# Kernel tuning notes

Measured on AMD Instinct MI355X. Metric: run time of the kernel, lower is better.

Reference implementation:

```python
import jax, jax.numpy as jnp
import numpy as np
import math

HEADS = 8
EMBED = 512
HEAD_DIM = EMBED // HEADS
N, L = 2, 256


def setup_inputs() -> dict:
    key = jax.random.key(0)
    ks = jax.random.split(key, 16)
    s = 0.05  # weight scale for numerical stability
    inp = {
        "values": jax.random.normal(ks[0], (N, L, EMBED), jnp.float32),
        "keys": jax.random.normal(ks[1], (N, L, EMBED), jnp.float32),
        "query": jax.random.normal(ks[2], (N, L, EMBED), jnp.float32),
        "pos": jax.random.normal(ks[3], (N, L, EMBED), jnp.float32),
        "rel": jax.random.normal(ks[4], (N, L, L, EMBED), jnp.float32),
        "mask": jnp.ones((N, L), jnp.float32),
        "Wv": jax.random.normal(ks[5], (HEAD_DIM, HEAD_DIM), jnp.float32) * s,
        "Wk": jax.random.normal(ks[6], (HEAD_DIM, HEAD_DIM), jnp.float32) * s,
        "Wq": jax.random.normal(ks[7], (HEAD_DIM, HEAD_DIM), jnp.float32) * s,
        "Wpq": jax.random.normal(ks[8], (HEAD_DIM, HEAD_DIM), jnp.float32) * s,
        "Wpk": jax.random.normal(ks[9], (HEAD_DIM, HEAD_DIM), jnp.float32) * s,
        "Wrk": jax.random.normal(ks[10], (HEAD_DIM, HEAD_DIM), jnp.float32) * s,
        "Wrq": jax.random.normal(ks[11], (HEAD_DIM, HEAD_DIM), jnp.float32) * s,
        "Wout": jax.random.normal(ks[12], (EMBED, EMBED), jnp.float32) * s,
        "bout": jnp.zeros((EMBED,), jnp.float32),
    }
    return inp


def reference(values, keys, query, pos, rel, mask, Wv, Wk, Wq, Wpq, Wpk, Wrk, Wrq, Wout, bout):
    n, lq, e = query.shape
    h, d = HEADS, e // HEADS
    # split heads; per-head Linear shares one [d,d] weight (y = x @ W.T)
    v = values.reshape(n, -1, h, d) @ Wv.T
    k = keys.reshape(n, -1, h, d) @ Wk.T
    q = query.reshape(n, lq, h, d) @ Wq.T
    p = pos.reshape(n, lq, h, d)
    r = rel.reshape(n, lq, lq, h, d)
    # mode == 'all': QK + pos-pos + two relative terms
    scores = jnp.einsum('nqhd,nkhd->nhqk', q, k)
    pq = p @ Wpq.T
    pk = p @ Wpk.T
    pos_scores = jnp.einsum('nqhd,nkhd->nhqk', pq, pk)
    rk = r @ Wrk.T
    rq = r @ Wrq.T
    rel1 = jnp.einsum('nqhd,nqkhd->nhqk', q, rk)
    rel2 = jnp.einsum('nqkhd,nkhd->nhqk', rq, k)
    energy = (scores + pos_scores + rel1 + rel2) / math.sqrt(2.0)
    energy = energy + (1.0 - mask)[:, None, None, :] * (-1e9)
    attn = jax.nn.softmax(energy, axis=3)
    out = jnp.einsum('nhqk,nkhd->nqhd', attn, v).reshape(n, lq, e)
    return out @ Wout.T + bout
```

## Files before the change

### kernel.cpp

```cpp
#include <hip/hip_runtime.h>
#include <hip/hip_bf16.h>

#define NB 2
#define L 256
#define H 8
#define D 64
#define E 512
#define NL (NB * L)
#define RSQRT2 0.70710678118654752f

__global__ __launch_bounds__(256) void k0_transpose(const float* __restrict__ Wout,
                                                    float* __restrict__ WoutT) {
    __shared__ float tile[64][65];
    int t = threadIdx.x;
    int bi = blockIdx.x >> 3;
    int bj = blockIdx.x & 7;
    int tx = t & 63, ty = t >> 6;
#pragma unroll
    for (int m = 0; m < 16; m++) {
        int el = ty + (m << 2);
        tile[el][tx] = Wout[(size_t)(bi * 64 + el) * E + bj * 64 + tx];
    }
    __syncthreads();
#pragma unroll
    for (int m = 0; m < 16; m++) {
        int cl = ty + (m << 2);
        WoutT[(size_t)(bj * 64 + cl) * E + bi * 64 + tx] = tile[tx][cl];
    }
}

__device__ __forceinline__ float dot64(const float* __restrict__ a,
                                       const float* __restrict__ w) {
    const float4* a4 = (const float4*)a;
    const float4* w4 = (const float4*)w;
    float acc = 0.f;
#pragma unroll
    for (int j = 0; j < 16; j++) {
        float4 x = a4[j], y = w4[j];
        acc = fmaf(x.x, y.x, acc);
        acc = fmaf(x.y, y.y, acc);
        acc = fmaf(x.z, y.z, acc);
        acc = fmaf(x.w, y.w, acc);
    }
    return acc;
}

__global__ __launch_bounds__(256) void k1_proj(
    const float* __restrict__ values, const float* __restrict__ keys,
    const float* __restrict__ query, const float* __restrict__ pos,
    const float* __restrict__ Wv, const float* __restrict__ Wk,
    const float* __restrict__ Wq, const float* __restrict__ Wpq,
    const float* __restrict__ Wpk, const float* __restrict__ Wrk,
    const float* __restrict__ Wrq,
    float* __restrict__ qv_ws, float* __restrict__ kv_ws,
    float* __restrict__ vv_ws, float* __restrict__ pq_ws,
    float* __restrict__ pk_ws, float* __restrict__ qrk_ws,
    float* __restrict__ krq_ws) {
    __shared__ float xq[E], xk[E], xv[E], xp[E];
    __shared__ float qs[E], ks[E];
    int t = threadIdx.x;
    int nl = blockIdx.x;
    size_t base = (size_t)nl * E;
    for (int j = t; j < E; j += 256) {
        xq[j] = query[base + j];
        xk[j] = keys[base + j];
        xv[j] = values[base + j];
        xp[j] = pos[base + j];
    }
    __syncthreads();
#pragma unroll
    for (int cc = 0; cc < 2; cc++) {
        int c = t + cc * 256;
        int h = c >> 6, i = c & 63;
        const float* xqh = xq + (h << 6);
        const float* xkh = xk + (h << 6);
        const float* xvh = xv + (h << 6);
        const float* xph = xp + (h << 6);
        float q_c = dot64(xqh, Wq + (i << 6));
        float k_c = dot64(xkh, Wk + (i << 6));
        float v_c = dot64(xvh, Wv + (i << 6));
        float pq_c = dot64(xph, Wpq + (i << 6));
        float pk_c = dot64(xph, Wpk + (i << 6));
        qv_ws[base + c] = q_c;
        kv_ws[base + c] = k_c;
        vv_ws[base + c] = v_c;
        pq_ws[base + c] = pq_c;
        pk_ws[base + c] = pk_c;
        qs[c] = q_c;
        ks[c] = k_c;
    }
    __syncthreads();
#pragma unroll
    for (int cc = 0; cc < 2; cc++) {
        int c = t + cc * 256;
        int h = c >> 6, d = c & 63;
        float aq = 0.f, ak = 0.f;
        const float* qh = qs + (h << 6);
        const float* kh = ks + (h << 6);
#pragma unroll 8
        for (int i = 0; i < 64; i++) {
            aq = fmaf(qh[i], Wrk[(i << 6) + d], aq);
            ak = fmaf(kh[i], Wrq[(i << 6) + d], ak);
        }
        qrk_ws[base + c] = aq;
        krq_ws[base + c] = ak;
    }
}

__global__ __launch_bounds__(256) void k2pre(
    const float* __restrict__ qv_ws, const float* __restrict__ kv_ws,
    const float* __restrict__ pq_ws, const float* __restrict__ pk_ws,
    const float* __restrict__ mask, float* __restrict__ e_ws) {
    __shared__ float qs[8 * 64], ps[8 * 64];
    int t = threadIdx.x;
    int b = blockIdx.x;
    int qt = b & 31;
    int h = (b >> 5) & 7;
    int n = b >> 8;
    int nb = n << 8;
    int q0 = qt << 3;
    int k = t;
#pragma unroll
    for (int it = 0; it < 2; it++) {
        int idx = t + (it << 8);
        int q = idx >> 6, d = idx & 63;
        size_t g = (size_t)(nb + q0 + q) * E + (h << 6) + d;
        qs[idx] = qv_ws[g];
        ps[idx] = pq_ws[g];
    }
    __syncthreads();
    const float4* kv4p = (const float4*)(kv_ws + (size_t)(nb + k) * E + (h << 6));
    const float4* pk4p = (const float4*)(pk_ws + (size_t)(nb + k) * E + (h << 6));
    float acc[8];
#pragma unroll
    for (int q = 0; q < 8; q++) acc[q] = 0.f;
#pragma unroll
    for (int d4 = 0; d4 < 16; d4++) {
        float4 kv4 = kv4p[d4];
        float4 pk4 = pk4p[d4];
#pragma unroll
        for (int q = 0; q < 8; q++) {
            float4 q4 = ((const float4*)qs)[(q << 4) + d4];
            float4 p4 = ((const float4*)ps)[(q << 4) + d4];
            float a = acc[q];
            a = fmaf(q4.x, kv4.x, a);
            a = fmaf(q4.y, kv4.y, a);
            a = fmaf(q4.z, kv4.z, a);
            a = fmaf(q4.w, kv4.w, a);
            a = fmaf(p4.x, pk4.x, a);
            a = fmaf(p4.y, pk4.y, a);
            a = fmaf(p4.z, pk4.z, a);
            a = fmaf(p4.w, pk4.w, a);
            acc[q] = a;
        }
    }
    float mk = (1.0f - mask[nb + k]) * (-1e9f);
#pragma unroll
    for (int q = 0; q < 8; q++) {
        e_ws[(size_t)(nb + q0 + q) * (H * L) + (h << 8) + k] = acc[q] * RSQRT2 + mk;
    }
}


#define K2REL_LOAD(R, QK, qi_)                                                  \
    do {                                                                        \
        const int gq_ = nbase + q0 + (qi_);                                     \
        const float* relb_ =                                                    \
            rel + (size_t)gq_ * (size_t)(L * E) + (size_t)kb * E + cq;          \
        _Pragma("unroll") for (int jj = 0; jj < 8; jj++)                        \
            R[jj] = *(const float4*)(relb_ + (size_t)((jj << 1) + rowsel) * E); \
        QK = *(const float4*)(qrk_ws + (size_t)gq_ * E + cq);                   \
    } while (0)

#define K2REL_COMP(R, QK, qi_)                                                  \
    do {                                                                        \
        const int gq_ = nbase + q0 + (qi_);                                     \
        float* rb_ = r_ws + (size_t)gq_ * (H * L) + (h << 8);                   \
        _Pragma("unroll") for (int jj = 0; jj < 8; jj++) {                      \
            float wx = QK.x + kq[jj].x;                                         \
            float wy = QK.y + kq[jj].y;                                         \
            float wz = QK.z + kq[jj].z;                                         \
            float ww = QK.w + kq[jj].w;                                         \
            float p = R[jj].x * wx;                                             \
            p = fmaf(R[jj].y, wy, p);                                           \
            p = fmaf(R[jj].z, wz, p);                                           \
            p = fmaf(R[jj].w, ww, p);                                           \
            p += __shfl_down(p, 8, 16);                                         \
            p += __shfl_down(p, 4, 16);                                         \
            p += __shfl_down(p, 2, 16);                                         \
            p += __shfl_down(p, 1, 16);                                         \
            if (sub == 0) rb_[kb + (jj << 1) + rowsel] = p * RSQRT2;            \
        }                                                                       \
    } while (0)

__global__ __launch_bounds__(256, 2) void k2rel(
    const float* __restrict__ rel, const float* __restrict__ qrk_ws,
    const float* __restrict__ krq_ws, float* __restrict__ r_ws) {
    int t = threadIdx.x;
    int b = blockIdx.x;
    int kc = b & 15;
    int qt = (b >> 4) & 15;
    int n = b >> 8;

    int lane128 = t & 127;
    int rowsel = t >> 7;
    int cq = lane128 << 2;
    int h = lane128 >> 4;
    int sub = t & 15;
    int nbase = n << 8;
    int kb = kc << 4;
    int q0 = qt << 4;

    float4 kq[8];
#pragma unroll
    for (int jj = 0; jj < 8; jj++) {
        kq[jj] = *(const float4*)(krq_ws +
                                  (size_t)(nbase + kb + (jj << 1) + rowsel) * E + cq);
    }

    float4 rA[8], rB[8], rC[8], rD[8];
    float4 qA, qB, qC, qD;
    K2REL_LOAD(rA, qA, 0);
    K2REL_LOAD(rB, qB, 1);
    K2REL_LOAD(rC, qC, 2);
#pragma unroll
    for (int qi = 0; qi < 16; qi += 4) {
        K2REL_LOAD(rD, qD, qi + 3);
        K2REL_COMP(rA, qA, qi);
        if (qi < 12) K2REL_LOAD(rA, qA, qi + 4);
        K2REL_COMP(rB, qB, qi + 1);
        if (qi < 12) K2REL_LOAD(rB, qB, qi + 5);
        K2REL_COMP(rC, qC, qi + 2);
        if (qi < 12) K2REL_LOAD(rC, qC, qi + 6);
        K2REL_COMP(rD, qD, qi + 3);
    }
}

__global__ __launch_bounds__(512) void k2b_soft_av(
    const float* __restrict__ e_ws, const float* __restrict__ r_ws,
    const float* __restrict__ vv_ws, float* __restrict__ attn_ws) {
    __shared__ float e_s[H * L];
    __shared__ float PS[4 * E];
    __shared__ float inv_s[H];
    int t = threadIdx.x;
    int nq = blockIdx.x;
    int n = nq >> 8;

    {
        float4 a = ((const float4*)(e_ws + (size_t)nq * (H * L)))[t];
        float4 b = ((const float4*)(r_ws + (size_t)nq * (H * L)))[t];
        a.x += b.x; a.y += b.y; a.z += b.z; a.w += b.w;
        ((float4*)e_s)[t] = a;
    }
    __syncthreads();

    {
        int hh = t >> 6;
        int lane = t & 63;
        float* eh = e_s + (hh << 8);
        float m = -INFINITY;
#pragma unroll
        for (int j = 0; j < 4; j++) m = fmaxf(m, eh[lane + (j << 6)]);
#pragma unroll
        for (int off = 32; off > 0; off >>= 1) m = fmaxf(m, __shfl_xor(m, off, 64));
        float s = 0.f;
#pragma unroll
        for (int j = 0; j < 4; j++) {
            int idx = lane + (j << 6);
            float ev = __expf(eh[idx] - m);
            eh[idx] = ev;
            s += ev;
        }
#pragma unroll
        for (int off = 32; off > 0; off >>= 1) s += __shfl_xor(s, off, 64);
        if (lane == 0) inv_s[hh] = 1.0f / s;
    }
    __syncthreads();

    {
        int c4 = (t & 127) << 2;
        int kseg = t >> 7;
        int h1 = c4 >> 6;
        const float* eh = e_s + (h1 << 8) + (kseg << 6);
        const float* vb = vv_ws + ((size_t)(n << 8) + (kseg << 6)) * E + c4;
        float4 acc = {0.f, 0.f, 0.f, 0.f};
#pragma unroll 16
        for (int k = 0; k < 64; k++) {
            float ev = eh[k];
            float4 v4 = *(const float4*)(vb + (size_t)k * E);
            acc.x = fmaf(ev, v4.x, acc.x);
            acc.y = fmaf(ev, v4.y, acc.y);
            acc.z = fmaf(ev, v4.z, acc.z);
            acc.w = fmaf(ev, v4.w, acc.w);
        }
        *(float4*)(PS + kseg * E + c4) = acc;
    }
    __syncthreads();

    {
        int c = t;
        float v = PS[c] + PS[E + c] + PS[2 * E + c] + PS[3 * E + c];
        attn_ws[(size_t)nq * E + c] = v * inv_s[t >> 6];
    }
}

__global__ __launch_bounds__(512) void k3_out(const float* __restrict__ attn_ws,
                                              const float* __restrict__ WoutT,
                                              const float* __restrict__ bout,
                                              float* __restrict__ out) {
    __shared__ float As[4 * E];
    int t = threadIdx.x;
    int r0 = blockIdx.x << 2;
    for (int j = t; j < 4 * E; j += 512) As[j] = attn_ws[(size_t)r0 * E + j];
    __syncthreads();
    float b0 = bout[t];
    float a0 = b0, a1 = b0, a2 = b0, a3 = b0;
#pragma unroll 8
    for (int c = 0; c < E; c++) {
        float w = WoutT[((size_t)c << 9) + t];
        a0 = fmaf(As[c], w, a0);
        a1 = fmaf(As[E + c], w, a1);
        a2 = fmaf(As[2 * E + c], w, a2);
        a3 = fmaf(As[3 * E + c], w, a3);
    }
    out[(size_t)(r0 + 0) * E + t] = a0;
    out[(size_t)(r0 + 1) * E + t] = a1;
    out[(size_t)(r0 + 2) * E + t] = a2;
    out[(size_t)(r0 + 3) * E + t] = a3;
}

extern "C" void kernel_launch(void* const* d_in, const int* in_sizes, int n_in,
                              void* d_out, int out_size, void* d_ws, size_t ws_size,
                              hipStream_t stream) {
    const float* values = (const float*)d_in[0];
    const float* keys = (const float*)d_in[1];
    const float* query = (const float*)d_in[2];
    const float* pos = (const float*)d_in[3];
    const float* rel = (const float*)d_in[4];
    const float* mask = (const float*)d_in[5];
    const float* Wv = (const float*)d_in[6];
    const float* Wk = (const float*)d_in[7];
    const float* Wq = (const float*)d_in[8];
    const float* Wpq = (const float*)d_in[9];
    const float* Wpk = (const float*)d_in[10];
    const float* Wrk = (const float*)d_in[11];
    const float* Wrq = (const float*)d_in[12];
    const float* Wout = (const float*)d_in[13];
    const float* bout = (const float*)d_in[14];
    float* out = (float*)d_out;

    float* ws = (float*)d_ws;
    const size_t SZ = (size_t)NL * E;
    float* qv_ws = ws + 0 * SZ;
    float* kv_ws = ws + 1 * SZ;
    float* vv_ws = ws + 2 * SZ;
    float* pq_ws = ws + 3 * SZ;
    float* pk_ws = ws + 4 * SZ;
    float* qrk_ws = ws + 5 * SZ;
    float* krq_ws = ws + 6 * SZ;
    float* attn_ws = ws + 7 * SZ;
    float* WoutT = ws + 8 * SZ;
    float* e_ws = ws + 9 * SZ;
    float* r_ws = e_ws + (size_t)NL * (H * L);

    k0_transpose<<<64, 256, 0, stream>>>(Wout, WoutT);
    k1_proj<<<NL, 256, 0, stream>>>(values, keys, query, pos, Wv, Wk, Wq, Wpq,
                                    Wpk, Wrk, Wrq, qv_ws, kv_ws, vv_ws, pq_ws,
                                    pk_ws, qrk_ws, krq_ws);
    k2pre<<<512, 256, 0, stream>>>(qv_ws, kv_ws, pq_ws, pk_ws, mask, e_ws);
    k2rel<<<512, 256, 0, stream>>>(rel, qrk_ws, krq_ws, r_ws);
    k2b_soft_av<<<NL, 512, 0, stream>>>(e_ws, r_ws, vv_ws, attn_ws);
    k3_out<<<NL / 4, 512, 0, stream>>>(attn_ws, WoutT, bout, out);
}
```

Measured before the change: 508.6 us.

## Fuse relative-position scoring with softmax and AV into one per-query kernel

Merges the rel-score kernel and the softmax/attention-V kernel into a single kernel with one block per (batch, query) row. The relative scores now stay in shared memory instead of going through a global r_ws buffer. This drops one launch and the r_ws round trip. In exchange, krq rows are reloaded per query rather than reused across 16 queries, and the AV stage runs on 256 threads instead of 512. The loop is also restructured to double-buffer rel and krq loads.

```diff
diff --git a/kernel.cpp b/kernel.cpp
--- a/kernel.cpp
+++ b/kernel.cpp
@@ -162,118 +162,102 @@
 }
 
 
-#define K2REL_LOAD(R, QK, qi_)                                                  \
-    do {                                                                        \
-        const int gq_ = nbase + q0 + (qi_);                                     \
-        const float* relb_ =                                                    \
-            rel + (size_t)gq_ * (size_t)(L * E) + (size_t)kb * E + cq;          \
-        _Pragma("unroll") for (int jj = 0; jj < 8; jj++)                        \
-            R[jj] = *(const float4*)(relb_ + (size_t)((jj << 1) + rowsel) * E); \
-        QK = *(const float4*)(qrk_ws + (size_t)gq_ * E + cq);                   \
+#define K2F_LOAD(RR, RK, b_)                                              \
+    do {                                                                  \
+        _Pragma("unroll") for (int jj = 0; jj < 8; jj++) {                \
+            int k_ = ((b_) << 4) + (jj << 1) + rowsel;                    \
+            RR[jj] = *(const float4*)(relb + ((size_t)k_ << 9) + cq);     \
+            RK[jj] = *(const float4*)(krqb + ((size_t)k_ << 9) + cq);     \
+        }                                                                 \
     } while (0)
 
-#define K2REL_COMP(R, QK, qi_)                                                  \
-    do {                                                                        \
-        const int gq_ = nbase + q0 + (qi_);                                     \
-        float* rb_ = r_ws + (size_t)gq_ * (H * L) + (h << 8);                   \
-        _Pragma("unroll") for (int jj = 0; jj < 8; jj++) {                      \
-            float wx = QK.x + kq[jj].x;                                         \
-            float wy = QK.y + kq[jj].y;                                         \
-            float wz = QK.z + kq[jj].z;                                         \
-            float ww = QK.w + kq[jj].w;                                         \
-            float p = R[jj].x * wx;                                             \
-            p = fmaf(R[jj].y, wy, p);                                           \
-            p = fmaf(R[jj].z, wz, p);                                           \
-            p = fmaf(R[jj].w, ww, p);                                           \
-            p += __shfl_down(p, 8, 16);                                         \
-            p += __shfl_down(p, 4, 16);                                         \
-            p += __shfl_down(p, 2, 16);                                         \
-            p += __shfl_down(p, 1, 16);                                         \
-            if (sub == 0) rb_[kb + (jj << 1) + rowsel] = p * RSQRT2;            \
-        }                                                                       \
+#define K2F_COMP(RR, RK, b_)                                              \
+    do {                                                                  \
+        _Pragma("unroll") for (int jj = 0; jj < 8; jj++) {                \
+            float wx = qrk4.x + RK[jj].x;                                 \
+            float wy = qrk4.y + RK[jj].y;                                 \
+            float wz = qrk4.z + RK[jj].z;                                 \
+            float ww = qrk4.w + RK[jj].w;                                 \
+            float p = RR[jj].x * wx;                                      \
+            p = fmaf(RR[jj].y, wy, p);                                    \
+            p = fmaf(RR[jj].z, wz, p);                                    \
+            p = fmaf(RR[jj].w, ww, p);                                    \
+            p += __shfl_down(p, 8, 16);                                   \
+            p += __shfl_down(p, 4, 16);                                   \
+            p += __shfl_down(p, 2, 16);                                   \
+            p += __shfl_down(p, 1, 16);                                   \
+            if (sub == 0) {                                               \
+                int k_ = ((b_) << 4) + (jj << 1) + rowsel;                \
+                r_s[(h << 8) + k_] = p * RSQRT2;                          \
+            }                                                             \
+        }                                                                 \
     } while (0)
 
-__global__ __launch_bounds__(256, 2) void k2rel(
+__global__ __launch_bounds__(256, 2) void k2f(
     const float* __restrict__ rel, const float* __restrict__ qrk_ws,
-    const float* __restrict__ krq_ws, float* __restrict__ r_ws) {
-    int t = threadIdx.x;
-    int b = blockIdx.x;
-    int kc = b & 15;
-    int qt = (b >> 4) & 15;
-    int n = b >> 8;
+    const float* __restrict__ krq_ws, const float* __restrict__ e_ws,
+    const float* __restrict__ vv_ws, float* __restrict__ attn_ws) {
+    __shared__ float e_s[H * L];
+    __shared__ float r_s[H * L];
+    __shared__ float PS[2 * E];
+    __shared__ float inv_s[H];
+    int t = threadIdx.x;
+    int nq = blockIdx.x;
+    int n = nq >> 8;
+
+    {
+        const float4* src = (const float4*)(e_ws + (size_t)nq * (H * L));
+        ((float4*)e_s)[t] = src[t];
+        ((float4*)e_s)[t + 256] = src[t + 256];
+    }
 
     int lane128 = t & 127;
     int rowsel = t >> 7;
     int cq = lane128 << 2;
     int h = lane128 >> 4;
     int sub = t & 15;
-    int nbase = n << 8;
-    int kb = kc << 4;
-    int q0 = qt << 4;
-
-    float4 kq[8];
-#pragma unroll
-    for (int jj = 0; jj < 8; jj++) {
-        kq[jj] = *(const float4*)(krq_ws +
-                                  (size_t)(nbase + kb + (jj << 1) + rowsel) * E + cq);
-    }
-
-    float4 rA[8], rB[8], rC[8], rD[8];
-    float4 qA, qB, qC, qD;
-    K2REL_LOAD(rA, qA, 0);
-    K2REL_LOAD(rB, qB, 1);
-    K2REL_LOAD(rC, qC, 2);
-#pragma unroll
-    for (int qi = 0; qi < 16; qi += 4) {
-        K2REL_LOAD(rD, qD, qi + 3);
-        K2REL_COMP(rA, qA, qi);
-        if (qi < 12) K2REL_LOAD(rA, qA, qi + 4);
-        K2REL_COMP(rB, qB, qi + 1);
-        if (qi < 12) K2REL_LOAD(rB, qB, qi + 5);
-        K2REL_COMP(rC, qC, qi + 2);
-        if (qi < 12) K2REL_LOAD(rC, qC, qi + 6);
-        K2REL_COMP(rD, qD, qi + 3);
-    }
-}
-
-__global__ __launch_bounds__(512) void k2b_soft_av(
-    const float* __restrict__ e_ws, const float* __restrict__ r_ws,
-    const float* __restrict__ vv_ws, float* __restrict__ attn_ws) {
-    __shared__ float e_s[H * L];
-    __shared__ float PS[4 * E];
-    __shared__ float inv_s[H];
-    int t = threadIdx.x;
-    int nq = blockIdx.x;
-    int n = nq >> 8;
+
+    const float* relb = rel + (((size_t)nq) << 8) * E;
+    const float* krqb = krq_ws + (((size_t)(n << 8))) * E;
+    float4 qrk4 = *(const float4*)(qrk_ws + (size_t)nq * E + cq);
+
+    float4 rAr[8], rAk[8], rBr[8], rBk[8];
+    K2F_LOAD(rAr, rAk, 0);
+#pragma unroll
+    for (int b = 0; b < 16; b += 2) {
+        K2F_LOAD(rBr, rBk, b + 1);
+        K2F_COMP(rAr, rAk, b);
+        if (b + 2 < 16) K2F_LOAD(rAr, rAk, b + 2);
+        K2F_COMP(rBr, rBk, b + 1);
+    }
+    __syncthreads();
 
     {
-        float4 a = ((const float4*)(e_ws + (size_t)nq * (H * L)))[t];
-        float4 b = ((const float4*)(r_ws + (size_t)nq * (H * L)))[t];
-        a.x += b.x; a.y += b.y; a.z += b.z; a.w += b.w;
-        ((float4*)e_s)[t] = a;
-    }
-    __syncthreads();
-
-    {
-        int hh = t >> 6;
-        int lane = t & 63;
+        int hh = t >> 5;
+        int l32 = t & 31;
         float* eh = e_s + (hh << 8);
+        const float* rh = r_s + (hh << 8);
+        float x[8];
         float m = -INFINITY;
 #pragma unroll
-        for (int j = 0; j < 4; j++) m = fmaxf(m, eh[lane + (j << 6)]);
-#pragma unroll
-        for (int off = 32; off > 0; off >>= 1) m = fmaxf(m, __shfl_xor(m, off, 64));
+        for (int j = 0; j < 8; j++) {
+            int idx = l32 + (j << 5);
+            x[j] = eh[idx] + rh[idx];
+            m = fmaxf(m, x[j]);
+        }
+#pragma unroll
+        for (int off = 16; off > 0; off >>= 1) m = fmaxf(m, __shfl_xor(m, off, 32));
         float s = 0.f;
 #pragma unroll
-        for (int j = 0; j < 4; j++) {
-            int idx = lane + (j << 6);
-            float ev = __expf(eh[idx] - m);
+        for (int j = 0; j < 8; j++) {
+            int idx = l32 + (j << 5);
+            float ev = __expf(x[j] - m);
             eh[idx] = ev;
             s += ev;
         }
 #pragma unroll
-        for (int off = 32; off > 0; off >>= 1) s += __shfl_xor(s, off, 64);
-        if (lane == 0) inv_s[hh] = 1.0f / s;
+        for (int off = 16; off > 0; off >>= 1) s += __shfl_xor(s, off, 32);
+        if (l32 == 0) inv_s[hh] = 1.0f / s;
     }
     __syncthreads();
 
@@ -281,13 +265,13 @@
         int c4 = (t & 127) << 2;
         int kseg = t >> 7;
         int h1 = c4 >> 6;
-        const float* eh = e_s + (h1 << 8) + (kseg << 6);
-        const float* vb = vv_ws + ((size_t)(n << 8) + (kseg << 6)) * E + c4;
+        const float* eh = e_s + (h1 << 8) + (kseg << 7);
+        const float* vb = vv_ws + ((size_t)((n << 8) + (kseg << 7))) * E + c4;
         float4 acc = {0.f, 0.f, 0.f, 0.f};
 #pragma unroll 16
-        for (int k = 0; k < 64; k++) {
+        for (int k = 0; k < 128; k++) {
             float ev = eh[k];
-            float4 v4 = *(const float4*)(vb + (size_t)k * E);
+            float4 v4 = *(const float4*)(vb + ((size_t)k << 9));
             acc.x = fmaf(ev, v4.x, acc.x);
             acc.y = fmaf(ev, v4.y, acc.y);
             acc.z = fmaf(ev, v4.z, acc.z);
@@ -298,9 +282,10 @@
     __syncthreads();
 
     {
-        int c = t;
-        float v = PS[c] + PS[E + c] + PS[2 * E + c] + PS[3 * E + c];
-        attn_ws[(size_t)nq * E + c] = v * inv_s[t >> 6];
+        float v0 = PS[t] + PS[E + t];
+        attn_ws[(size_t)nq * E + t] = v0 * inv_s[t >> 6];
+        float v1 = PS[256 + t] + PS[E + 256 + t];
+        attn_ws[(size_t)nq * E + 256 + t] = v1 * inv_s[(256 + t) >> 6];
     }
 }
 
@@ -361,14 +346,12 @@
     float* attn_ws = ws + 7 * SZ;
     float* WoutT = ws + 8 * SZ;
     float* e_ws = ws + 9 * SZ;
-    float* r_ws = e_ws + (size_t)NL * (H * L);
 
     k0_transpose<<<64, 256, 0, stream>>>(Wout, WoutT);
     k1_proj<<<NL, 256, 0, stream>>>(values, keys, query, pos, Wv, Wk, Wq, Wpq,
                                     Wpk, Wrk, Wrq, qv_ws, kv_ws, vv_ws, pq_ws,
                                     pk_ws, qrk_ws, krq_ws);
     k2pre<<<512, 256, 0, stream>>>(qv_ws, kv_ws, pq_ws, pk_ws, mask, e_ws);
-    k2rel<<<512, 256, 0, stream>>>(rel, qrk_ws, krq_ws, r_ws);
-    k2b_soft_av<<<NL, 512, 0, stream>>>(e_ws, r_ws, vv_ws, attn_ws);
+    k2f<<<512, 256, 0, stream>>>(rel, qrk_ws, krq_ws, e_ws, vv_ws, attn_ws);
     k3_out<<<NL / 4, 512, 0, stream>>>(attn_ws, WoutT, bout, out);
 }
```

Result: faster. 494.1 us (-2.8%).
